# Optimization experiments

Measured on AMD Instinct MI355X. Metric: run time of the kernel, lower is better.

Reference implementation:

```python
import jax, jax.numpy as jnp
import numpy as np

IN_FEATURES = 256
OUT_FEATURES = 256
GRID_SIZE = 5
SPLINE_ORDER = 3  # k


def setup_inputs() -> dict:
    key = jax.random.key(0)
    k1, k2, k3, k4 = jax.random.split(key, 4)
    x = jax.random.uniform(k1, (1024, IN_FEATURES), dtype=jnp.float32)  # in [0,1) subset of grid_range
    base_weight = jax.random.normal(k2, (IN_FEATURES, OUT_FEATURES), dtype=jnp.float32) * 0.05
    n_basis = GRID_SIZE + SPLINE_ORDER - 1  # 7
    spline_weight = jax.random.normal(k3, (IN_FEATURES, OUT_FEATURES, n_basis), dtype=jnp.float32) * 0.05
    # grid: (grid_size, in_features); sorted per feature inside grid_range (-1,1)
    grid = jnp.sort(jax.random.uniform(k4, (GRID_SIZE, IN_FEATURES), dtype=jnp.float32, minval=-1.0, maxval=1.0), axis=0)
    return {"x": x, "base_weight": base_weight, "spline_weight": spline_weight, "grid": grid}


def _safe_div(num, den):
    # B-spline convention: 0/0 terms contribute 0 (repeated knots from constant-fill grid extension).
    ok = den != 0
    return jnp.where(ok, num / jnp.where(ok, den, 1.0), 0.0)


def _bspline_basis(x, grid, k):
    # x: (b, in); grid: (G, in) -> basis (b, in, G+k-1) via Cox-de Boor recursion.
    gt = grid.T  # (in, G)
    left = jnp.repeat(2.0 * gt[:, :1] - gt[:, k:k + 1], k, axis=1)       # k copies of 2*g0 - g_k
    right = jnp.repeat(2.0 * gt[:, -1:] - gt[:, -k - 1:-k], k, axis=1)   # k copies of 2*g_-1 - g_{-k-1}
    eg = jnp.concatenate([left, gt, right], axis=1)  # (in, G+2k) extended grid
    xe = x[:, :, None]  # (b, in, 1)
    B = ((xe >= eg[None, :, :-1]) & (xe < eg[None, :, 1:])).astype(x.dtype)  # order-1 indicator basis
    for d in range(1, k):
        lt = _safe_div(xe - eg[None, :, :-d - 1], (eg[:, d:-1] - eg[:, :-d - 1])[None])
        rt = _safe_div(eg[None, :, d + 1:] - xe, (eg[:, d + 1:] - eg[:, 1:-d])[None])
        B = lt * B[..., :-1] + rt * B[..., 1:]
    return B[..., :grid.shape[0] + k - 1]  # first G+k-1 functions, matching spline_weight's last dim


def reference(x, base_weight, spline_weight, grid):
    k = SPLINE_ORDER
    basis = _bspline_basis(x, grid, k)                     # (b, in, K)
    base_out = x @ base_weight                             # (b, out)
    spline_out = jnp.einsum('bik,iok->bio', basis, spline_weight)  # (b, in, out)
    # base_out (b,out) broadcasts against (b,in,out), as in the original tf code
    return jax.nn.silu(base_out[:, None, :] + spline_out)
```

## Files before the change

### kernel.cpp

```cpp
#include <hip/hip_runtime.h>
#include <math.h>


#define NF 256
#define BCH 16
#define ICH 16

typedef float f32x4 __attribute__((ext_vector_type(4)));

__device__ __forceinline__ float silu_f(float z) {
    float e = __expf(-z);
    return z * __builtin_amdgcn_rcpf(1.0f + e);
}

__global__ __launch_bounds__(256) void base_gemm(const float* __restrict__ x,
                                                 const float* __restrict__ W,
                                                 float* __restrict__ base) {
    __shared__ float xs[4][NF];
    const int b0 = blockIdx.x * 4;
    const int t = threadIdx.x;
    {
        const int row = t >> 6;
        const int c4 = (t & 63) * 4;
        *reinterpret_cast<f32x4*>(&xs[row][c4]) =
            *reinterpret_cast<const f32x4*>(&x[(size_t)(b0 + row) * NF + c4]);
    }
    __syncthreads();
    float acc0 = 0.f, acc1 = 0.f, acc2 = 0.f, acc3 = 0.f;
#pragma unroll 8
    for (int k = 0; k < NF; ++k) {
        float w = W[k * NF + t];
        acc0 += xs[0][k] * w;
        acc1 += xs[1][k] * w;
        acc2 += xs[2][k] * w;
        acc3 += xs[3][k] * w;
    }
    base[(size_t)(b0 + 0) * NF + t] = acc0;
    base[(size_t)(b0 + 1) * NF + t] = acc1;
    base[(size_t)(b0 + 2) * NF + t] = acc2;
    base[(size_t)(b0 + 3) * NF + t] = acc3;
}

__global__ __launch_bounds__(256) void kan_main(const float* __restrict__ x,
                                                const float* __restrict__ sw,
                                                const float* __restrict__ grid,
                                                const float* __restrict__ base,
                                                float* __restrict__ out) {
    const int i0 = blockIdx.x * ICH;
    const int b0 = blockIdx.y * BCH;
    const int tid = threadIdx.x;

    __shared__ float bas[ICH][BCH][8];
    __shared__ float base_s[BCH][NF];

#pragma unroll
    for (int r = 0; r < 4; ++r) {
        const int f4 = tid + r * 256;
        const int row = f4 >> 6;
        const int c4 = (f4 & 63) * 4;
        *reinterpret_cast<f32x4*>(&base_s[row][c4]) =
            *reinterpret_cast<const f32x4*>(&base[(size_t)(b0 + row) * NF + c4]);
    }

    {
        const int ii = tid & (ICH - 1);
        const int bb = tid >> 4;
        const int gi = i0 + ii;
        const float xv = x[(size_t)(b0 + bb) * NF + gi];
        const float g0 = grid[0 * NF + gi];
        const float g1 = grid[1 * NF + gi];
        const float g2 = grid[2 * NF + gi];
        const float g3 = grid[3 * NF + gi];
        const float g4 = grid[4 * NF + gi];
        const float L = 2.f * g0 - g3;
        const float R = 2.f * g4 - g1;
        float eg[11] = {L, L, L, g0, g1, g2, g3, g4, R, R, R};

        float B0[10];
#pragma unroll
        for (int t = 0; t < 10; ++t)
            B0[t] = (xv >= eg[t] && xv < eg[t + 1]) ? 1.f : 0.f;
        float B1[9];
#pragma unroll
        for (int t = 0; t < 9; ++t) {
            float dl = eg[t + 1] - eg[t];
            float dr = eg[t + 2] - eg[t + 1];
            float lt = (dl != 0.f) ? (xv - eg[t]) / dl : 0.f;
            float rt = (dr != 0.f) ? (eg[t + 2] - xv) / dr : 0.f;
            B1[t] = lt * B0[t] + rt * B0[t + 1];
        }
        float B2[8];
#pragma unroll
        for (int t = 0; t < 8; ++t) {
            float dl = eg[t + 2] - eg[t];
            float dr = eg[t + 3] - eg[t + 1];
            float lt = (dl != 0.f) ? (xv - eg[t]) / dl : 0.f;
            float rt = (dr != 0.f) ? (eg[t + 3] - xv) / dr : 0.f;
            B2[t] = lt * B1[t] + rt * B1[t + 1];
        }
#pragma unroll
        for (int k = 0; k < 7; ++k) bas[ii][bb][k] = B2[k];
        bas[ii][bb][7] = 0.f;
    }

    __syncthreads();

    const int lane = tid & 63;
    const int wv = tid >> 6;

    for (int step = 0; step < 4; ++step) {
        const int ii = step * 4 + wv;
        const int i = i0 + ii;

        f32x4 q[7];
        const f32x4* p4 = reinterpret_cast<const f32x4*>(
            &sw[((size_t)i * NF + lane * 4) * 7]);
#pragma unroll
        for (int j = 0; j < 7; ++j) q[j] = p4[j];
        float s[28];
#pragma unroll
        for (int j = 0; j < 7; ++j) {
            s[j * 4 + 0] = q[j].x; s[j * 4 + 1] = q[j].y;
            s[j * 4 + 2] = q[j].z; s[j * 4 + 3] = q[j].w;
        }

        float* op = out + ((size_t)b0 * NF + i) * NF + lane * 4;

#pragma unroll
        for (int bb = 0; bb < BCH; ++bb) {
            f32x4 bl = *reinterpret_cast<const f32x4*>(&bas[ii][bb][0]);
            f32x4 bh = *reinterpret_cast<const f32x4*>(&bas[ii][bb][4]);
            const float bk[7] = {bl.x, bl.y, bl.z, bl.w, bh.x, bh.y, bh.z};
            f32x4 bs = *reinterpret_cast<const f32x4*>(&base_s[bb][lane * 4]);
            float a0 = bs.x, a1 = bs.y, a2 = bs.z, a3 = bs.w;
#pragma unroll
            for (int k = 0; k < 7; ++k) {
                a0 += bk[k] * s[0 * 7 + k];
                a1 += bk[k] * s[1 * 7 + k];
                a2 += bk[k] * s[2 * 7 + k];
                a3 += bk[k] * s[3 * 7 + k];
            }
            f32x4 o4;
            o4.x = silu_f(a0);
            o4.y = silu_f(a1);
            o4.z = silu_f(a2);
            o4.w = silu_f(a3);
            *reinterpret_cast<f32x4*>(op + (size_t)bb * NF * NF) = o4;
        }
    }
}

extern "C" void kernel_launch(void* const* d_in, const int* in_sizes, int n_in,
                              void* d_out, int out_size, void* d_ws, size_t ws_size,
                              hipStream_t stream) {
    const float* x    = (const float*)d_in[0];
    const float* bw   = (const float*)d_in[1];
    const float* sw   = (const float*)d_in[2];
    const float* grid = (const float*)d_in[3];
    float* out = (float*)d_out;
    float* base = (float*)d_ws;

    base_gemm<<<dim3(256), 256, 0, stream>>>(x, bw, base);
    kan_main<<<dim3(16, 64), 256, 0, stream>>>(x, sw, grid, base, out);
}
```

Baseline: 65.23 us.

## Fuse base GEMM into main KAN kernel with per-block batch rows

Merges the base linear GEMM and the spline/SiLU kernel into a single launch. Each 512-thread block takes 4 batch rows, computes their base outputs and all B-spline bases in shared memory, then streams the full spline weight tensor across all input features. This drops one launch and the workspace round trip for the base output. In exchange, every block now rereads the entire 1.8 MB spline weight tensor and the 256 KB base weight (from L2), and the grid is only 256 blocks.

```diff
diff --git a/kernel.cpp b/kernel.cpp
--- a/kernel.cpp
+++ b/kernel.cpp
@@ -3,8 +3,8 @@
 
 
 #define NF 256
-#define BCH 16
-#define ICH 16
+#define BROWS 4
+#define G 4
 
 typedef float f32x4 __attribute__((ext_vector_type(4)));
 
@@ -13,139 +13,138 @@
     return z * __builtin_amdgcn_rcpf(1.0f + e);
 }
 
-__global__ __launch_bounds__(256) void base_gemm(const float* __restrict__ x,
-                                                 const float* __restrict__ W,
-                                                 float* __restrict__ base) {
-    __shared__ float xs[4][NF];
-    const int b0 = blockIdx.x * 4;
-    const int t = threadIdx.x;
-    {
-        const int row = t >> 6;
-        const int c4 = (t & 63) * 4;
+__global__ __launch_bounds__(512, 2) void kan_fused(const float* __restrict__ x,
+                                                    const float* __restrict__ W,
+                                                    const float* __restrict__ sw,
+                                                    const float* __restrict__ grid,
+                                                    float* __restrict__ out) {
+    const int b0 = blockIdx.x * BROWS;
+    const int tid = threadIdx.x;
+
+    __shared__ float xs[BROWS][NF];
+    __shared__ float base_s[BROWS][NF];
+    __shared__ float bas[BROWS][NF][8];
+
+    if (tid < 256) {
+        const int row = tid >> 6;
+        const int c4 = (tid & 63) * 4;
         *reinterpret_cast<f32x4*>(&xs[row][c4]) =
             *reinterpret_cast<const f32x4*>(&x[(size_t)(b0 + row) * NF + c4]);
     }
     __syncthreads();
-    float acc0 = 0.f, acc1 = 0.f, acc2 = 0.f, acc3 = 0.f;
-#pragma unroll 8
-    for (int k = 0; k < NF; ++k) {
-        float w = W[k * NF + t];
-        acc0 += xs[0][k] * w;
-        acc1 += xs[1][k] * w;
-        acc2 += xs[2][k] * w;
-        acc3 += xs[3][k] * w;
-    }
-    base[(size_t)(b0 + 0) * NF + t] = acc0;
-    base[(size_t)(b0 + 1) * NF + t] = acc1;
-    base[(size_t)(b0 + 2) * NF + t] = acc2;
-    base[(size_t)(b0 + 3) * NF + t] = acc3;
-}
 
-__global__ __launch_bounds__(256) void kan_main(const float* __restrict__ x,
-                                                const float* __restrict__ sw,
-                                                const float* __restrict__ grid,
-                                                const float* __restrict__ base,
-                                                float* __restrict__ out) {
-    const int i0 = blockIdx.x * ICH;
-    const int b0 = blockIdx.y * BCH;
-    const int tid = threadIdx.x;
-
-    __shared__ float bas[ICH][BCH][8];
-    __shared__ float base_s[BCH][NF];
-
-#pragma unroll
-    for (int r = 0; r < 4; ++r) {
-        const int f4 = tid + r * 256;
-        const int row = f4 >> 6;
-        const int c4 = (f4 & 63) * 4;
-        *reinterpret_cast<f32x4*>(&base_s[row][c4]) =
-            *reinterpret_cast<const f32x4*>(&base[(size_t)(b0 + row) * NF + c4]);
+    {
+        const int o = tid & 255;
+        const int h = tid >> 8;
+        float acc0 = 0.f, acc1 = 0.f;
+#pragma unroll 16
+        for (int k = 0; k < NF; ++k) {
+            const float w = W[k * NF + o];
+            acc0 += xs[2 * h + 0][k] * w;
+            acc1 += xs[2 * h + 1][k] * w;
+        }
+        base_s[2 * h + 0][o] = acc0;
+        base_s[2 * h + 1][o] = acc1;
     }
 
     {
-        const int ii = tid & (ICH - 1);
-        const int bb = tid >> 4;
-        const int gi = i0 + ii;
-        const float xv = x[(size_t)(b0 + bb) * NF + gi];
-        const float g0 = grid[0 * NF + gi];
-        const float g1 = grid[1 * NF + gi];
-        const float g2 = grid[2 * NF + gi];
-        const float g3 = grid[3 * NF + gi];
-        const float g4 = grid[4 * NF + gi];
+        const int i = tid & 255;
+        const int hh = tid >> 8;
+        const float g0 = grid[0 * NF + i];
+        const float g1 = grid[1 * NF + i];
+        const float g2 = grid[2 * NF + i];
+        const float g3 = grid[3 * NF + i];
+        const float g4 = grid[4 * NF + i];
         const float L = 2.f * g0 - g3;
         const float R = 2.f * g4 - g1;
-        float eg[11] = {L, L, L, g0, g1, g2, g3, g4, R, R, R};
+        const float eg[11] = {L, L, L, g0, g1, g2, g3, g4, R, R, R};
 
-        float B0[10];
 #pragma unroll
-        for (int t = 0; t < 10; ++t)
-            B0[t] = (xv >= eg[t] && xv < eg[t + 1]) ? 1.f : 0.f;
-        float B1[9];
+        for (int rep = 0; rep < 2; ++rep) {
+            const int bb = hh + 2 * rep;
+            const float xv = xs[bb][i];
+
+            float B0[10];
 #pragma unroll
-        for (int t = 0; t < 9; ++t) {
-            float dl = eg[t + 1] - eg[t];
-            float dr = eg[t + 2] - eg[t + 1];
-            float lt = (dl != 0.f) ? (xv - eg[t]) / dl : 0.f;
-            float rt = (dr != 0.f) ? (eg[t + 2] - xv) / dr : 0.f;
-            B1[t] = lt * B0[t] + rt * B0[t + 1];
+            for (int t = 0; t < 10; ++t)
+                B0[t] = (xv >= eg[t] && xv < eg[t + 1]) ? 1.f : 0.f;
+            float B1[9];
+#pragma unroll
+            for (int t = 0; t < 9; ++t) {
+                const float dl = eg[t + 1] - eg[t];
+                const float dr = eg[t + 2] - eg[t + 1];
+                const float lt = (dl != 0.f) ? (xv - eg[t]) / dl : 0.f;
+                const float rt = (dr != 0.f) ? (eg[t + 2] - xv) / dr : 0.f;
+                B1[t] = lt * B0[t] + rt * B0[t + 1];
+            }
+            float B2[8];
+#pragma unroll
+            for (int t = 0; t < 8; ++t) {
+                const float dl = eg[t + 2] - eg[t];
+                const float dr = eg[t + 3] - eg[t + 1];
+                const float lt = (dl != 0.f) ? (xv - eg[t]) / dl : 0.f;
+                const float rt = (dr != 0.f) ? (eg[t + 3] - xv) / dr : 0.f;
+                B2[t] = lt * B1[t] + rt * B1[t + 1];
+            }
+#pragma unroll
+            for (int k = 0; k < 7; ++k) bas[bb][i][k] = B2[k];
+            bas[bb][i][7] = 0.f;
         }
-        float B2[8];
-#pragma unroll
-        for (int t = 0; t < 8; ++t) {
-            float dl = eg[t + 2] - eg[t];
-            float dr = eg[t + 3] - eg[t + 1];
-            float lt = (dl != 0.f) ? (xv - eg[t]) / dl : 0.f;
-            float rt = (dr != 0.f) ? (eg[t + 3] - xv) / dr : 0.f;
-            B2[t] = lt * B1[t] + rt * B1[t + 1];
-        }
-#pragma unroll
-        for (int k = 0; k < 7; ++k) bas[ii][bb][k] = B2[k];
-        bas[ii][bb][7] = 0.f;
     }
-
     __syncthreads();
 
     const int lane = tid & 63;
     const int wv = tid >> 6;
+    const int o4 = lane * 4;
 
-    for (int step = 0; step < 4; ++step) {
-        const int ii = step * 4 + wv;
-        const int i = i0 + ii;
+    f32x4 bs[BROWS];
+#pragma unroll
+    for (int bb = 0; bb < BROWS; ++bb)
+        bs[bb] = *reinterpret_cast<const f32x4*>(&base_s[bb][o4]);
 
-        f32x4 q[7];
-        const f32x4* p4 = reinterpret_cast<const f32x4*>(
-            &sw[((size_t)i * NF + lane * 4) * 7]);
+    for (int gs = 0; gs < NF / (8 * G); ++gs) {
+        f32x4 q[G][7];
 #pragma unroll
-        for (int j = 0; j < 7; ++j) q[j] = p4[j];
-        float s[28];
+        for (int j = 0; j < G; ++j) {
+            const int i = (gs * G + j) * 8 + wv;
+            const f32x4* p4 =
+                reinterpret_cast<const f32x4*>(&sw[((size_t)i * NF + o4) * 7]);
 #pragma unroll
-        for (int j = 0; j < 7; ++j) {
-            s[j * 4 + 0] = q[j].x; s[j * 4 + 1] = q[j].y;
-            s[j * 4 + 2] = q[j].z; s[j * 4 + 3] = q[j].w;
+            for (int kk = 0; kk < 7; ++kk) q[j][kk] = p4[kk];
         }
 
-        float* op = out + ((size_t)b0 * NF + i) * NF + lane * 4;
-
 #pragma unroll
-        for (int bb = 0; bb < BCH; ++bb) {
-            f32x4 bl = *reinterpret_cast<const f32x4*>(&bas[ii][bb][0]);
-            f32x4 bh = *reinterpret_cast<const f32x4*>(&bas[ii][bb][4]);
-            const float bk[7] = {bl.x, bl.y, bl.z, bl.w, bh.x, bh.y, bh.z};
-            f32x4 bs = *reinterpret_cast<const f32x4*>(&base_s[bb][lane * 4]);
-            float a0 = bs.x, a1 = bs.y, a2 = bs.z, a3 = bs.w;
+        for (int bb = 0; bb < BROWS; ++bb) {
 #pragma unroll
-            for (int k = 0; k < 7; ++k) {
-                a0 += bk[k] * s[0 * 7 + k];
-                a1 += bk[k] * s[1 * 7 + k];
-                a2 += bk[k] * s[2 * 7 + k];
-                a3 += bk[k] * s[3 * 7 + k];
+            for (int j = 0; j < G; ++j) {
+                const int i = (gs * G + j) * 8 + wv;
+                const f32x4 bl = *reinterpret_cast<const f32x4*>(&bas[bb][i][0]);
+                const f32x4 bh = *reinterpret_cast<const f32x4*>(&bas[bb][i][4]);
+                const float bk[7] = {bl.x, bl.y, bl.z, bl.w, bh.x, bh.y, bh.z};
+                float s[28];
+#pragma unroll
+                for (int m = 0; m < 7; ++m) {
+                    s[m * 4 + 0] = q[j][m].x;
+                    s[m * 4 + 1] = q[j][m].y;
+                    s[m * 4 + 2] = q[j][m].z;
+                    s[m * 4 + 3] = q[j][m].w;
+                }
+                float a0 = bs[bb].x, a1 = bs[bb].y, a2 = bs[bb].z, a3 = bs[bb].w;
+#pragma unroll
+                for (int k = 0; k < 7; ++k) {
+                    a0 += bk[k] * s[0 * 7 + k];
+                    a1 += bk[k] * s[1 * 7 + k];
+                    a2 += bk[k] * s[2 * 7 + k];
+                    a3 += bk[k] * s[3 * 7 + k];
+                }
+                f32x4 o4v;
+                o4v.x = silu_f(a0);
+                o4v.y = silu_f(a1);
+                o4v.z = silu_f(a2);
+                o4v.w = silu_f(a3);
+                *reinterpret_cast<f32x4*>(
+                    &out[((size_t)(b0 + bb) * NF + i) * NF + o4]) = o4v;
             }
-            f32x4 o4;
-            o4.x = silu_f(a0);
-            o4.y = silu_f(a1);
-            o4.z = silu_f(a2);
-            o4.w = silu_f(a3);
-            *reinterpret_cast<f32x4*>(op + (size_t)bb * NF * NF) = o4;
         }
     }
 }
@@ -158,8 +157,6 @@
     const float* sw   = (const float*)d_in[2];
     const float* grid = (const float*)d_in[3];
     float* out = (float*)d_out;
-    float* base = (float*)d_ws;
 
-    base_gemm<<<dim3(256), 256, 0, stream>>>(x, bw, base);
-    kan_main<<<dim3(16, 64), 256, 0, stream>>>(x, sw, grid, base, out);
+    kan_fused<<<dim3(256), 512, 0, stream>>>(x, bw, sw, grid, out);
 }
```

Result: slower. 74.15 us (+13.7%).
